# Kernel optimization log

Measured on AMD Instinct MI355X. Metric: run time of the kernel, lower is better.

The kernel has to match this reference:

```python
import jax, jax.numpy as jnp
import numpy as np

DIM = 1024
HEADS = 16
HEAD_DIM = DIM // HEADS


def setup_inputs() -> dict:
    key = jax.random.key(0)
    ks = jax.random.split(key, 9)
    s = 1.0 / np.sqrt(DIM)
    return {
        "x": jax.random.normal(ks[0], (2, 2048, DIM), dtype=jnp.float32),
        "Wq": jax.random.normal(ks[1], (DIM, DIM), dtype=jnp.float32) * s,
        "bq": jnp.zeros((DIM,), dtype=jnp.float32),
        "Wk": jax.random.normal(ks[2], (DIM, DIM), dtype=jnp.float32) * s,
        "bk": jnp.zeros((DIM,), dtype=jnp.float32),
        "Wv": jax.random.normal(ks[3], (DIM, DIM), dtype=jnp.float32) * s,
        "bv": jnp.zeros((DIM,), dtype=jnp.float32),
        "Wo": jax.random.normal(ks[4], (DIM, DIM), dtype=jnp.float32) * s,
        "bo": jnp.zeros((DIM,), dtype=jnp.float32),
    }


def reference(x, Wq, bq, Wk, bk, Wv, bv, Wo, bo):
    B, S, D = x.shape
    H, Dh = HEADS, HEAD_DIM

    def split_heads(t):  # (B,S,D) -> (B,H,S,Dh)
        return t.reshape(B, S, H, Dh).transpose(0, 2, 1, 3)

    q = split_heads(x @ Wq + bq)
    k = split_heads(x @ Wk + bk)
    v = split_heads(x @ Wv + bv)

    scores = jnp.einsum("bhsd,bhtd->bhst", q, k) / np.sqrt(Dh).astype(x.dtype)
    attn = jax.nn.softmax(scores, axis=-1)
    ctx = jnp.einsum("bhst,bhtd->bhsd", attn, v)
    ctx = ctx.transpose(0, 2, 1, 3).reshape(B, S, D)
    return ctx @ Wo + bo
```

## Files before the change

kernel.cpp:

```cpp
#include <hip/hip_runtime.h>
#include <hip/hip_bf16.h>
#include <cstdint>

typedef __bf16 bf16;
typedef __bf16 bf16x8 __attribute__((ext_vector_type(8)));
typedef float f32x4 __attribute__((ext_vector_type(4)));
typedef float f32x8 __attribute__((ext_vector_type(8)));
typedef float f32x16 __attribute__((ext_vector_type(16)));

#define DIM   1024
#define SEQ   2048
#define BATCH 2
#define HEADS 16
#define HDIM  64

#define QSCALE 0.1803368801111204f

__device__ __forceinline__ void gload_lds16(const void* g, void* l) {
    __builtin_amdgcn_global_load_lds(
        (const __attribute__((address_space(1))) void*)g,
        (__attribute__((address_space(3))) void*)l,
        16, 0, 0);
}

__device__ __forceinline__ uint32_t pkbf(float a, float b) {
    union { bf16 h[2]; uint32_t u; } t;
    t.h[0] = (bf16)a; t.h[1] = (bf16)b;
    return t.u;
}

#define LO8(v)  __builtin_shufflevector(v, v, 0, 1, 2, 3, 4, 5, 6, 7)
#define HI8(v)  __builtin_shufflevector(v, v, 8, 9, 10, 11, 12, 13, 14, 15)
#define LO4(v)  __builtin_shufflevector(v, v, 0, 1, 2, 3)
#define HI4(v)  __builtin_shufflevector(v, v, 4, 5, 6, 7)

__global__ __launch_bounds__(256) void cvt_wt_kernel(const float* __restrict__ Wq,
                                                     const float* __restrict__ Wk,
                                                     const float* __restrict__ Wv,
                                                     const float* __restrict__ Wo,
                                                     bf16* __restrict__ Wt) {
    int z = blockIdx.z;
    const float* W = (z == 0) ? Wq : (z == 1) ? Wk : (z == 2) ? Wv : Wo;
    bf16* out = Wt + (size_t)z * DIM * DIM;
    int w = threadIdx.x >> 6, lane = threadIdx.x & 63;
    int n  = blockIdx.x * 64 + lane;
    int kb = blockIdx.y * 32 + w * 8;
    bf16x8 o;
#pragma unroll
    for (int j = 0; j < 8; ++j)
        o[j] = (bf16)W[(size_t)(kb + j) * DIM + n];
    *(bf16x8*)(out + (size_t)n * DIM + kb) = o;
}

template <int MODE>
__global__ __launch_bounds__(256) void gemm128_kernel(
        const void* __restrict__ Ap,
        const bf16* __restrict__ WtB,
        const float* __restrict__ b0,
        const float* __restrict__ b1,
        const float* __restrict__ b2,
        void* __restrict__ outp) {
    constexpr int K  = DIM;
    constexpr int BN = (MODE == 1) ? 64 : 128;
    constexpr int NR = BN / 32;
    int z = (MODE == 0) ? blockIdx.z : 0;
    const bf16* Bt = WtB + (size_t)z * DIM * DIM;
    const float* bias = (MODE == 0) ? ((z == 0) ? b0 : (z == 1) ? b1 : b2) : b0;

    int m0 = blockIdx.y * 128, n0 = blockIdx.x * BN;
    int tid = threadIdx.x;
    int w = tid >> 6, lane = tid & 63, l15 = lane & 15, l4 = lane >> 4;
    int wr = (w >> 1) * 64, wc = (w & 1) * (BN / 2);

    __shared__ __align__(16) bf16 As[128 * 32];
    __shared__ __align__(16) bf16 Bs[BN * 32];

    int arow = tid >> 1, acol = (tid & 1) * 16;
    const float* asrc = (MODE == 0)
        ? (const float*)Ap + (size_t)(m0 + arow) * K + acol : nullptr;

    f32x4 acc[4][NR] = {};

    for (int k0 = 0; k0 < K; k0 += 32) {
#pragma unroll
        for (int rr = 0; rr < BN / 64; ++rr) {
            int c = rr * 256 + tid;
            gload_lds16(Bt + (size_t)(n0 + (c >> 2)) * K + k0 + (c & 3) * 8, &Bs[c * 8]);
        }
        if constexpr (MODE == 0) {
            const float4* s4 = (const float4*)(asrc + k0);
            float4 f0 = s4[0], f1 = s4[1], f2 = s4[2], f3 = s4[3];
            bf16x8 e0, e1;
            e0[0] = (bf16)f0.x; e0[1] = (bf16)f0.y; e0[2] = (bf16)f0.z; e0[3] = (bf16)f0.w;
            e0[4] = (bf16)f1.x; e0[5] = (bf16)f1.y; e0[6] = (bf16)f1.z; e0[7] = (bf16)f1.w;
            e1[0] = (bf16)f2.x; e1[1] = (bf16)f2.y; e1[2] = (bf16)f2.z; e1[3] = (bf16)f2.w;
            e1[4] = (bf16)f3.x; e1[5] = (bf16)f3.y; e1[6] = (bf16)f3.z; e1[7] = (bf16)f3.w;
            *(bf16x8*)&As[arow * 32 + acol]     = e0;
            *(bf16x8*)&As[arow * 32 + acol + 8] = e1;
        } else {
            const bf16* A = (const bf16*)Ap;
#pragma unroll
            for (int rr = 0; rr < 2; ++rr) {
                int c = rr * 256 + tid;
                gload_lds16(A + (size_t)(m0 + (c >> 2)) * K + k0 + (c & 3) * 8, &As[c * 8]);
            }
        }
        __syncthreads();
        bf16x8 af[4], bfr[NR];
#pragma unroll
        for (int m = 0; m < 4; ++m)
            af[m] = *(const bf16x8*)&As[(wr + m * 16 + l15) * 32 + l4 * 8];
#pragma unroll
        for (int n = 0; n < NR; ++n)
            bfr[n] = *(const bf16x8*)&Bs[(wc + n * 16 + l15) * 32 + l4 * 8];
#pragma unroll
        for (int m = 0; m < 4; ++m)
#pragma unroll
            for (int n = 0; n < NR; ++n)
                acc[m][n] = __builtin_amdgcn_mfma_f32_16x16x32_bf16(
                    af[m], bfr[n], acc[m][n], 0, 0, 0);
        __syncthreads();
    }

    float oscale = (MODE == 0 && z == 0) ? QSCALE : 1.0f;
#pragma unroll
    for (int n = 0; n < NR; ++n) {
        int col = n0 + wc + n * 16 + l15;
        float bv = bias[col];
#pragma unroll
        for (int m = 0; m < 4; ++m) {
            int rowb = m0 + wr + m * 16 + l4 * 4;
            if (MODE == 1) {
                float* out = (float*)outp;
#pragma unroll
                for (int i = 0; i < 4; ++i)
                    out[(size_t)(rowb + i) * DIM + col] = acc[m][n][i] + bv;
            } else if (z < 2) {
                bf16* out = (bf16*)outp + (size_t)z * (BATCH * HEADS * SEQ * HDIM);
                int h = col >> 6, d = col & 63;
#pragma unroll
                for (int i = 0; i < 4; ++i) {
                    int row = rowb + i;
                    int bb = row >> 11, s = row & 2047;
                    out[(((size_t)(bb * HEADS + h)) * SEQ + s) * HDIM + d] =
                        (bf16)((acc[m][n][i] + bv) * oscale);
                }
            } else {
                bf16* out = (bf16*)outp + (size_t)2 * (BATCH * HEADS * SEQ * HDIM);
                int h = col >> 6, d = col & 63;
                int bb = rowb >> 11, s0 = rowb & 2047;
                union { bf16 hh[4]; ushort4 v; } pk;
#pragma unroll
                for (int i = 0; i < 4; ++i) pk.hh[i] = (bf16)(acc[m][n][i] + bv);
                *(ushort4*)&out[(((size_t)(bb * HEADS + h)) * HDIM + d) * SEQ + s0] = pk.v;
            }
        }
    }
}

__global__ __launch_bounds__(256) void attn_kernel(const bf16* __restrict__ Q,
                                                   const bf16* __restrict__ K,
                                                   const bf16* __restrict__ Vt,
                                                   bf16* __restrict__ ctx) {
    int bid = blockIdx.x;
    int xcd = bid & 7, i = bid >> 3;
    int hb  = xcd * (BATCH * HEADS / 8) + (i >> 4);
    int q0  = (i & 15) * 128;
    int bb = hb >> 4, h = hb & 15;
    int tid = threadIdx.x, w = tid >> 6, lane = tid & 63;
    int l31 = lane & 31, hi = lane >> 5;

    const bf16* Qh = Q  + (size_t)hb * SEQ * HDIM;
    const bf16* Kh = K  + (size_t)hb * SEQ * HDIM;
    const bf16* Vh = Vt + (size_t)hb * HDIM * SEQ;

    __shared__ __align__(16) bf16 Ks[2][8192];
    __shared__ __align__(16) bf16 Vs[2][8192];

    int qrow = q0 + w * 32 + l31;
    bf16x8 qf[4];
#pragma unroll
    for (int ks = 0; ks < 4; ++ks)
        qf[ks] = *(const bf16x8*)&Qh[(size_t)qrow * HDIM + ks * 16 + hi * 8];

    f32x16 o0 = {}, o1 = {};
    float l = 0.f;

    const bf16* kbase[2];
    const bf16* vbase[2];
    int ldsoff[2];
#pragma unroll
    for (int r = 0; r < 2; ++r) {
        int c = r * 256 + tid;
        int krow = c >> 3, kj = (c & 7) ^ (krow & 7);
        kbase[r] = Kh + (size_t)krow * HDIM + kj * 8;
        int dh = (c >> 3) & 63, vj = (c & 7) ^ (dh & 7);
        vbase[r] = Vh + (size_t)dh * SEQ + vj * 8;
        ldsoff[r] = c * 8;
    }
    auto stage = [&](bf16* ksd, bf16* vsd, int kv0) {
#pragma unroll
        for (int r = 0; r < 2; ++r) {
            gload_lds16(kbase[r] + (size_t)kv0 * HDIM,        ksd + ldsoff[r]);
            gload_lds16(kbase[r] + (size_t)(kv0 + 64) * HDIM, ksd + ldsoff[r] + 4096);
            gload_lds16(vbase[r] + kv0,                       vsd + ldsoff[r]);
            gload_lds16(vbase[r] + kv0 + 64,                  vsd + ldsoff[r] + 4096);
        }
    };

    int koffA = l31 * 128;
    int cb[4];
#pragma unroll
    for (int ks = 0; ks < 4; ++ks)
        cb[ks] = ((2 * ks + hi) ^ (l31 & 7)) << 4;

    auto sub64 = [&](const char* kp, const char* vp) {
        f32x16 s0 = {}, s1 = {};
        __builtin_amdgcn_s_setprio(1);
#pragma unroll
        for (int ks = 0; ks < 4; ++ks) {
            bf16x8 k0 = *(const bf16x8*)(kp + koffA + cb[ks]);
            bf16x8 k1 = *(const bf16x8*)(kp + koffA + 4096 + cb[ks]);
            s0 = __builtin_amdgcn_mfma_f32_32x32x16_bf16(k0, qf[ks], s0, 0, 0, 0);
            s1 = __builtin_amdgcn_mfma_f32_32x32x16_bf16(k1, qf[ks], s1, 0, 0, 0);
        }
        __builtin_amdgcn_s_setprio(0);

#pragma unroll
        for (int r = 0; r < 16; ++r) {
            s0[r] = __builtin_amdgcn_exp2f(s0[r]);
            s1[r] = __builtin_amdgcn_exp2f(s1[r]);
        }

        f32x16 a16 = s0 + s1;
        f32x8  a8  = LO8(a16) + HI8(a16);
        f32x4  a4  = LO4(a8) + HI4(a8);
        l += (a4[0] + a4[1]) + (a4[2] + a4[3]);

        bf16x8 pa[4];
#pragma unroll
        for (int f2 = 0; f2 < 4; ++f2) {
            const f32x16& s = (f2 < 2) ? s0 : s1;
            int rb = (f2 & 1) * 8;
            uint32_t w0 = pkbf(s[rb + 0], s[rb + 1]), w1 = pkbf(s[rb + 2], s[rb + 3]);
            uint32_t w2 = pkbf(s[rb + 4], s[rb + 5]), w3 = pkbf(s[rb + 6], s[rb + 7]);
            asm("v_permlane32_swap_b32 %0, %1" : "+v"(w0), "+v"(w2));
            asm("v_permlane32_swap_b32 %0, %1" : "+v"(w1), "+v"(w3));
            union { uint32_t u[4]; bf16x8 v; } t2;
            t2.u[0] = w0; t2.u[1] = w1; t2.u[2] = w2; t2.u[3] = w3;
            pa[f2] = t2.v;
        }

        __builtin_amdgcn_s_setprio(1);
#pragma unroll
        for (int ks = 0; ks < 4; ++ks) {
            bf16x8 v0 = *(const bf16x8*)(vp + koffA + cb[ks]);
            bf16x8 v1 = *(const bf16x8*)(vp + koffA + 4096 + cb[ks]);
            o0 = __builtin_amdgcn_mfma_f32_32x32x16_bf16(v0, pa[ks], o0, 0, 0, 0);
            o1 = __builtin_amdgcn_mfma_f32_32x32x16_bf16(v1, pa[ks], o1, 0, 0, 0);
        }
        __builtin_amdgcn_s_setprio(0);
    };

    auto proc = [&](const char* ksb, const char* vsb) {
        sub64(ksb, vsb);
        sub64(ksb + 8192, vsb + 8192);
    };

    constexpr int NT = SEQ / 128;
    stage(Ks[0], Vs[0], 0);
    __syncthreads();

    for (int t = 0; t < NT; t += 2) {
        if (t + 1 < NT) stage(Ks[1], Vs[1], (t + 1) * 128);
        proc((const char*)&Ks[0][0], (const char*)&Vs[0][0]);
        __syncthreads();
        if (t + 2 < NT) stage(Ks[0], Vs[0], (t + 2) * 128);
        proc((const char*)&Ks[1][0], (const char*)&Vs[1][0]);
        __syncthreads();
    }

    l += __shfl_xor(l, 32);
    float inv = 1.0f / l;
    size_t base = ((size_t)bb * SEQ + qrow) * DIM + h * HDIM;
#pragma unroll
    for (int g = 0; g < 4; ++g) {
        int dh0 = 8 * g + 4 * hi;
        union { bf16 hh[4]; ushort4 u; } a, b2;
#pragma unroll
        for (int i = 0; i < 4; ++i) {
            a.hh[i]  = (bf16)(o0[4 * g + i] * inv);
            b2.hh[i] = (bf16)(o1[4 * g + i] * inv);
        }
        *(ushort4*)&ctx[base + dh0]      = a.u;
        *(ushort4*)&ctx[base + 32 + dh0] = b2.u;
    }
}

extern "C" void kernel_launch(void* const* d_in, const int* in_sizes, int n_in,
                              void* d_out, int out_size, void* d_ws, size_t ws_size,
                              hipStream_t stream) {
    const float* x  = (const float*)d_in[0];
    const float* Wq = (const float*)d_in[1];
    const float* bq = (const float*)d_in[2];
    const float* Wk = (const float*)d_in[3];
    const float* bk = (const float*)d_in[4];
    const float* Wv = (const float*)d_in[5];
    const float* bv = (const float*)d_in[6];
    const float* Wo = (const float*)d_in[7];
    const float* bo = (const float*)d_in[8];

    char* ws = (char*)d_ws;
    bf16* Wt  = (bf16*)(ws + (8u  << 20));
    bf16* Qb  = (bf16*)(ws + (16u << 20));
    bf16* Kb  = (bf16*)(ws + (24u << 20));
    bf16* Vb  = (bf16*)(ws + (32u << 20));
    bf16* ctx = (bf16*)(ws + (40u << 20));

    cvt_wt_kernel<<<dim3(16, 32, 4), 256, 0, stream>>>(Wq, Wk, Wv, Wo, Wt);
    gemm128_kernel<0><<<dim3(8, 32, 3), 256, 0, stream>>>(x, Wt, bq, bk, bv, (void*)Qb);
    attn_kernel<<<512, 256, 0, stream>>>(Qb, Kb, Vb, ctx);
    gemm128_kernel<1><<<dim3(16, 32), 256, 0, stream>>>(
        ctx, Wt + (size_t)3 * DIM * DIM, bo, bo, bo, (void*)d_out);
}
```

Measured before the change: 120.6 us.

## Store V in MFMA fragment layout and load directly from global in attention

The projection GEMM writes V in a pre-swizzled layout matching the MFMA operand fragment, so each lane loads 16 contiguous bytes per fragment. The attention kernel drops V staging through LDS and reads V fragments directly from global memory inside the inner loop. This halves LDS usage and LDS traffic and removes the V async copies. In exchange, the four waves of a block redundantly fetch the same V data from cache, and global latency sits on the critical path without explicit prefetching.

```diff
diff --git a/kernel.cpp b/kernel.cpp
--- a/kernel.cpp
+++ b/kernel.cpp
@@ -146,13 +146,19 @@
                         (bf16)((acc[m][n][i] + bv) * oscale);
                 }
             } else {
-                bf16* out = (bf16*)outp + (size_t)2 * (BATCH * HEADS * SEQ * HDIM);
+                char* out = (char*)outp + (size_t)2 * (BATCH * HEADS * SEQ * HDIM) * 2;
                 int h = col >> 6, d = col & 63;
+                int dblk = d >> 5;
                 int bb = rowb >> 11, s0 = rowb & 2047;
+                int hb2 = bb * HEADS + h;
+                int lane2 = (d & 31) + 32 * ((s0 >> 3) & 1);
+                size_t off = (size_t)(hb2 * 64 + (s0 >> 5)) * 4096
+                             + (dblk * 2 + ((s0 >> 4) & 1)) * 1024
+                             + lane2 * 16 + (s0 & 7) * 2;
                 union { bf16 hh[4]; ushort4 v; } pk;
 #pragma unroll
                 for (int i = 0; i < 4; ++i) pk.hh[i] = (bf16)(acc[m][n][i] + bv);
-                *(ushort4*)&out[(((size_t)(bb * HEADS + h)) * HDIM + d) * SEQ + s0] = pk.v;
+                *(ushort4*)(out + off) = pk.v;
             }
         }
     }
@@ -160,7 +166,7 @@
 
 __global__ __launch_bounds__(256) void attn_kernel(const bf16* __restrict__ Q,
                                                    const bf16* __restrict__ K,
-                                                   const bf16* __restrict__ Vt,
+                                                   const bf16* __restrict__ Vf,
                                                    bf16* __restrict__ ctx) {
     int bid = blockIdx.x;
     int xcd = bid & 7, i = bid >> 3;
@@ -170,12 +176,11 @@
     int tid = threadIdx.x, w = tid >> 6, lane = tid & 63;
     int l31 = lane & 31, hi = lane >> 5;
 
-    const bf16* Qh = Q  + (size_t)hb * SEQ * HDIM;
-    const bf16* Kh = K  + (size_t)hb * SEQ * HDIM;
-    const bf16* Vh = Vt + (size_t)hb * HDIM * SEQ;
+    const bf16* Qh = Q + (size_t)hb * SEQ * HDIM;
+    const bf16* Kh = K + (size_t)hb * SEQ * HDIM;
+    const char* Vh = (const char*)Vf + (size_t)hb * 64 * 4096 + lane * 16;
 
     __shared__ __align__(16) bf16 Ks[2][8192];
-    __shared__ __align__(16) bf16 Vs[2][8192];
 
     int qrow = q0 + w * 32 + l31;
     bf16x8 qf[4];
@@ -187,24 +192,19 @@
     float l = 0.f;
 
     const bf16* kbase[2];
-    const bf16* vbase[2];
     int ldsoff[2];
 #pragma unroll
     for (int r = 0; r < 2; ++r) {
         int c = r * 256 + tid;
         int krow = c >> 3, kj = (c & 7) ^ (krow & 7);
         kbase[r] = Kh + (size_t)krow * HDIM + kj * 8;
-        int dh = (c >> 3) & 63, vj = (c & 7) ^ (dh & 7);
-        vbase[r] = Vh + (size_t)dh * SEQ + vj * 8;
         ldsoff[r] = c * 8;
     }
-    auto stage = [&](bf16* ksd, bf16* vsd, int kv0) {
+    auto stage = [&](bf16* ksd, int kv0) {
 #pragma unroll
         for (int r = 0; r < 2; ++r) {
             gload_lds16(kbase[r] + (size_t)kv0 * HDIM,        ksd + ldsoff[r]);
             gload_lds16(kbase[r] + (size_t)(kv0 + 64) * HDIM, ksd + ldsoff[r] + 4096);
-            gload_lds16(vbase[r] + kv0,                       vsd + ldsoff[r]);
-            gload_lds16(vbase[r] + kv0 + 64,                  vsd + ldsoff[r] + 4096);
         }
     };
 
@@ -214,7 +214,7 @@
     for (int ks = 0; ks < 4; ++ks)
         cb[ks] = ((2 * ks + hi) ^ (l31 & 7)) << 4;
 
-    auto sub64 = [&](const char* kp, const char* vp) {
+    auto sub64 = [&](const char* kp, const char* vjp) {
         f32x16 s0 = {}, s1 = {};
         __builtin_amdgcn_s_setprio(1);
 #pragma unroll
@@ -225,6 +225,15 @@
             s1 = __builtin_amdgcn_mfma_f32_32x32x16_bf16(k1, qf[ks], s1, 0, 0, 0);
         }
         __builtin_amdgcn_s_setprio(0);
+
+        bf16x8 v0 = *(const bf16x8*)(vjp);
+        bf16x8 v1 = *(const bf16x8*)(vjp + 1024);
+        bf16x8 v2 = *(const bf16x8*)(vjp + 2048);
+        bf16x8 v3 = *(const bf16x8*)(vjp + 3072);
+        bf16x8 v4 = *(const bf16x8*)(vjp + 4096);
+        bf16x8 v5 = *(const bf16x8*)(vjp + 5120);
+        bf16x8 v6 = *(const bf16x8*)(vjp + 6144);
+        bf16x8 v7 = *(const bf16x8*)(vjp + 7168);
 
 #pragma unroll
         for (int r = 0; r < 16; ++r) {
@@ -252,31 +261,32 @@
         }
 
         __builtin_amdgcn_s_setprio(1);
-#pragma unroll
-        for (int ks = 0; ks < 4; ++ks) {
-            bf16x8 v0 = *(const bf16x8*)(vp + koffA + cb[ks]);
-            bf16x8 v1 = *(const bf16x8*)(vp + koffA + 4096 + cb[ks]);
-            o0 = __builtin_amdgcn_mfma_f32_32x32x16_bf16(v0, pa[ks], o0, 0, 0, 0);
-            o1 = __builtin_amdgcn_mfma_f32_32x32x16_bf16(v1, pa[ks], o1, 0, 0, 0);
-        }
+        o0 = __builtin_amdgcn_mfma_f32_32x32x16_bf16(v0, pa[0], o0, 0, 0, 0);
+        o0 = __builtin_amdgcn_mfma_f32_32x32x16_bf16(v1, pa[1], o0, 0, 0, 0);
+        o1 = __builtin_amdgcn_mfma_f32_32x32x16_bf16(v2, pa[0], o1, 0, 0, 0);
+        o1 = __builtin_amdgcn_mfma_f32_32x32x16_bf16(v3, pa[1], o1, 0, 0, 0);
+        o0 = __builtin_amdgcn_mfma_f32_32x32x16_bf16(v4, pa[2], o0, 0, 0, 0);
+        o0 = __builtin_amdgcn_mfma_f32_32x32x16_bf16(v5, pa[3], o0, 0, 0, 0);
+        o1 = __builtin_amdgcn_mfma_f32_32x32x16_bf16(v6, pa[2], o1, 0, 0, 0);
+        o1 = __builtin_amdgcn_mfma_f32_32x32x16_bf16(v7, pa[3], o1, 0, 0, 0);
         __builtin_amdgcn_s_setprio(0);
     };
 
-    auto proc = [&](const char* ksb, const char* vsb) {
-        sub64(ksb, vsb);
-        sub64(ksb + 8192, vsb + 8192);
+    auto proc = [&](const char* ksb, int kv0) {
+        sub64(ksb,        Vh + (size_t)(kv0 >> 5) * 4096);
+        sub64(ksb + 8192, Vh + (size_t)((kv0 + 64) >> 5) * 4096);
     };
 
     constexpr int NT = SEQ / 128;
-    stage(Ks[0], Vs[0], 0);
+    stage(Ks[0], 0);
     __syncthreads();
 
     for (int t = 0; t < NT; t += 2) {
-        if (t + 1 < NT) stage(Ks[1], Vs[1], (t + 1) * 128);
-        proc((const char*)&Ks[0][0], (const char*)&Vs[0][0]);
+        if (t + 1 < NT) stage(Ks[1], (t + 1) * 128);
+        proc((const char*)&Ks[0][0], t * 128);
         __syncthreads();
-        if (t + 2 < NT) stage(Ks[0], Vs[0], (t + 2) * 128);
-        proc((const char*)&Ks[1][0], (const char*)&Vs[1][0]);
+        if (t + 2 < NT) stage(Ks[0], (t + 2) * 128);
+        proc((const char*)&Ks[1][0], (t + 1) * 128);
         __syncthreads();
     }
 
@@ -314,12 +324,12 @@
     bf16* Wt  = (bf16*)(ws + (8u  << 20));
     bf16* Qb  = (bf16*)(ws + (16u << 20));
     bf16* Kb  = (bf16*)(ws + (24u << 20));
-    bf16* Vb  = (bf16*)(ws + (32u << 20));
+    bf16* Vf  = (bf16*)(ws + (32u << 20));
     bf16* ctx = (bf16*)(ws + (40u << 20));
 
     cvt_wt_kernel<<<dim3(16, 32, 4), 256, 0, stream>>>(Wq, Wk, Wv, Wo, Wt);
     gemm128_kernel<0><<<dim3(8, 32, 3), 256, 0, stream>>>(x, Wt, bq, bk, bv, (void*)Qb);
-    attn_kernel<<<512, 256, 0, stream>>>(Qb, Kb, Vb, ctx);
+    attn_kernel<<<512, 256, 0, stream>>>(Qb, Kb, Vf, ctx);
     gemm128_kernel<1><<<dim3(16, 32), 256, 0, stream>>>(
         ctx, Wt + (size_t)3 * DIM * DIM, bo, bo, bo, (void*)d_out);
 }
```

Result: no change. 121.3 us (+0.6%).
